# Kernel optimization log

Measured on AMD Instinct MI355X. Metric: run time of the kernel, lower is better.

The kernel has to match this reference:

```python
import jax, jax.numpy as jnp
import numpy as np

KH = KW = 3
PAD = 1
STRIDE = 1
C_IN = 32
C_OUT = 16
H = W = 64
B = 64
H_OUT = (H - KH + 2 * PAD) // STRIDE + 1
W_OUT = (W - KW + 2 * PAD) // STRIDE + 1
S = H_OUT * W_OUT
K = C_IN * KH * KW


def unfold_2d(x):
    # x: [B, C, H, W] -> [B, C*KH*KW, S], torch.nn.functional.unfold ordering
    xp = jnp.pad(x, ((0, 0), (0, 0), (PAD, PAD), (PAD, PAD)))
    patches = []
    for i in range(KH):
        for j in range(KW):
            patches.append(xp[:, :, i:i + H_OUT * STRIDE:STRIDE, j:j + W_OUT * STRIDE:STRIDE])
    u = jnp.stack(patches, axis=2)  # [B, C, KH*KW, H_OUT, W_OUT]
    return u.reshape(x.shape[0], K, S)


def setup_inputs() -> dict:
    key = jax.random.key(0)
    k1, k2, k3 = jax.random.split(key, 3)
    X = jax.random.normal(k1, (B, C_IN, H, W), dtype=jnp.float32)
    # kaiming normal (linear): std = 1/sqrt(fan_in), fan_in = K for each location's GEMM
    weight = jax.random.normal(k2, (S, K, C_OUT), dtype=jnp.float32) / jnp.sqrt(jnp.float32(K))
    # xavier uniform over [H_OUT, W_OUT]
    lim = np.sqrt(6.0 / (H_OUT + W_OUT))
    bias = jax.random.uniform(k3, (H_OUT, W_OUT), dtype=jnp.float32, minval=-lim, maxval=lim)
    return {"X": X, "weight": weight, "bias": bias}


def reference(X, weight, bias):
    ufld = unfold_2d(X)                               # [B, K, S]
    ufld = ufld + bias.reshape(1, 1, -1)              # bias added per-location to patches
    h = jnp.einsum('bks,skc->bcs', ufld, weight)      # per-location unshared GEMM
    return h.reshape(X.shape[0], C_OUT, H_OUT, W_OUT)
```

## Files before the change

### kernel.cpp

```cpp
#include <hip/hip_runtime.h>
#include <stdint.h>
#include <stddef.h>

#define HOUT 64
#define WOUT 64
#define CIN  32
#define COUT 16
#define BATCH 64
#define SLOC 4096
#define KTOT 288
#define HPAD 66

typedef __attribute__((ext_vector_type(8))) short  short8;
typedef __attribute__((ext_vector_type(4))) float  floatx4;

static __device__ __forceinline__ unsigned short f2bf(float f) {
    union { float f; unsigned int u; } v; v.f = f;
    unsigned int u = v.u;
    unsigned int r = (u + 0x7FFFu + ((u >> 16) & 1u)) >> 16;
    return (unsigned short)r;
}

__global__ __launch_bounds__(256) void zero_border_kernel(unsigned short* __restrict__ xt) {
    int bid = blockIdx.x;
    int h1, w1;
    if (bid < 66)       { h1 = 0;  w1 = bid; }
    else if (bid < 132) { h1 = 65; w1 = bid - 66; }
    else { int r = bid - 132; h1 = (r >> 1) + 1; w1 = (r & 1) ? 65 : 0; }
    uint4* dst = (uint4*)(xt + (size_t)(h1 * HPAD + w1) * 2048);
    dst[threadIdx.x] = uint4{0u, 0u, 0u, 0u};
}

__global__ __launch_bounds__(256) void transpose_kernel(const float* __restrict__ X,
                                                        unsigned short* __restrict__ xt) {
    int h = blockIdx.x;
    int b = blockIdx.y;
    int t = threadIdx.x;
    int w  = t >> 2;
    int cg = t & 3;

    const float* xb = X + (((size_t)b * CIN + cg * 8) * HOUT + h) * WOUT + w;
    unsigned short v[8];
#pragma unroll
    for (int j = 0; j < 8; ++j)
        v[j] = f2bf(xb[(size_t)j * HOUT * WOUT]);

    uint4 pack;
    pack.x = (unsigned)v[0] | ((unsigned)v[1] << 16);
    pack.y = (unsigned)v[2] | ((unsigned)v[3] << 16);
    pack.z = (unsigned)v[4] | ((unsigned)v[5] << 16);
    pack.w = (unsigned)v[6] | ((unsigned)v[7] << 16);

    *(uint4*)(xt + (size_t)((h + 1) * HPAD + (w + 1)) * 2048 + b * CIN + cg * 8) = pack;
}

__global__ __launch_bounds__(576) void wprep_kernel(const float* __restrict__ Wg,
                                                    const float* __restrict__ bias,
                                                    uint4* __restrict__ wt,
                                                    float* __restrict__ bsum) {
    __shared__ float red[9][16];
    int s    = blockIdx.x;
    int t    = threadIdx.x >> 6;
    int lane = threadIdx.x & 63;
    int q = lane >> 4, n = lane & 15;

    const float* wb = Wg + (size_t)s * (KTOT * COUT) + (size_t)((8 * q) * 9 + t) * COUT + n;
    float w[8];
#pragma unroll
    for (int j = 0; j < 8; ++j)
        w[j] = wb[(size_t)j * 9 * COUT];

    float csum = 0.f;
    unsigned short h[8];
#pragma unroll
    for (int j = 0; j < 8; ++j) { csum += w[j]; h[j] = f2bf(w[j]); }

    uint4 pack;
    pack.x = (unsigned)h[0] | ((unsigned)h[1] << 16);
    pack.y = (unsigned)h[2] | ((unsigned)h[3] << 16);
    pack.z = (unsigned)h[4] | ((unsigned)h[5] << 16);
    pack.w = (unsigned)h[6] | ((unsigned)h[7] << 16);
    wt[(size_t)(s * 9 + t) * 64 + lane] = pack;

    csum += __shfl_xor(csum, 16, 64);
    csum += __shfl_xor(csum, 32, 64);
    if (lane < 16) red[t][n] = csum;
    __syncthreads();
    if (threadIdx.x < 16) {
        float tot = 0.f;
#pragma unroll
        for (int tt = 0; tt < 9; ++tt) tot += red[tt][threadIdx.x];
        bsum[s * COUT + threadIdx.x] = bias[s] * tot;
    }
}

__global__ __launch_bounds__(256, 4) void varconv_kernel(const unsigned short* __restrict__ xt,
                                                         const uint4* __restrict__ wt,
                                                         const float* __restrict__ bsum,
                                                         float* __restrict__ out) {
    __shared__ float lds[16 * 16 * 16];

    int id = blockIdx.x;
    int lo = id & 7;
    int q4 = (id >> 3) & 3;
    int g  = ((id >> 5) << 3) | lo;
    int s0 = g * 16;
    int y  = s0 >> 6;
    int x0 = s0 & 63;
    int B0 = q4 * 16;

    int lane = threadIdx.x & 63, wv = threadIdx.x >> 6;
    int q = lane >> 4;
    int n = lane & 15;

#pragma unroll
    for (int i = 0; i < 4; ++i) {
        int sl = wv * 4 + i;
        int s  = s0 + sl;
        int x  = x0 + sl;

        const uint4* wf = wt + (size_t)s * 9 * 64 + lane;
        short8 bf[9];
#pragma unroll
        for (int t = 0; t < 9; ++t)
            bf[t] = *(const short8*)(wf + t * 64);

        float badd = bsum[s * COUT + n];

        const unsigned short* ab = xt + (size_t)(B0 + n) * CIN + q * 8;
        short8 af[9];
#pragma unroll
        for (int t = 0; t < 9; ++t) {
            const int cy = t / 3, cx = t % 3;
            af[t] = *(const short8*)(ab + (size_t)((y + cy) * HPAD + (x + cx)) * 2048);
        }

        floatx4 acc = {0.f, 0.f, 0.f, 0.f};
#pragma unroll
        for (int t = 0; t < 9; ++t)
            acc = __builtin_amdgcn_mfma_f32_16x16x32_bf16(af[t], bf[t], acc, 0, 0, 0);

        int slot = q ^ (n & 3);
        floatx4 v = {acc[0] + badd, acc[1] + badd, acc[2] + badd, acc[3] + badd};
        *(floatx4*)&lds[n * 256 + sl * 16 + slot * 4] = v;
    }

    __syncthreads();

    int c   = lane >> 2;
    int slg = lane & 3;
#pragma unroll
    for (int i2 = 0; i2 < 4; ++i2) {
        int ib   = wv * 4 + i2;
        int slot = (ib >> 2) ^ (c & 3);
        float o0[4];
#pragma unroll
        for (int e = 0; e < 4; ++e)
            o0[e] = lds[c * 256 + (slg * 4 + e) * 16 + slot * 4 + (ib & 3)];
        floatx4 o = {o0[0], o0[1], o0[2], o0[3]};
        *(floatx4*)(out + ((size_t)((B0 + ib) * COUT + c)) * SLOC + s0 + slg * 4) = o;
    }
}

extern "C" void kernel_launch(void* const* d_in, const int* in_sizes, int n_in,
                              void* d_out, int out_size, void* d_ws, size_t ws_size,
                              hipStream_t stream) {
    const float* X    = (const float*)d_in[0];
    const float* Wg   = (const float*)d_in[1];
    const float* bias = (const float*)d_in[2];
    float* out = (float*)d_out;

    unsigned short* xt = (unsigned short*)d_ws;
    uint4* wt   = (uint4*)((char*)d_ws + 17842176);
    float* bsum = (float*)((char*)d_ws + 17842176 + 37748736);

    zero_border_kernel<<<260, 256, 0, stream>>>(xt);
    transpose_kernel<<<dim3(64, 64), 256, 0, stream>>>(X, xt);
    wprep_kernel<<<SLOC, 576, 0, stream>>>(Wg, bias, wt, bsum);
    varconv_kernel<<<1024, 256, 0, stream>>>(xt, wt, bsum, out);
}
```

Measured before the change: 165.2 us.

## Fuse border-zero, transpose and weight-prep kernels into one prep kernel; pad LDS rows

Merges the three preprocessing kernels (border zeroing, input transpose to bf16, weight packing with bias sums) into a single 1024-block kernel. Each block now does four transpose units and one wave per weight location, with the bias column sum reduced by wave shuffles instead of an LDS reduction. The goal is to cut launch overhead and the tiny-block inefficiency of the separate kernels. Separately, the output-staging LDS tile gets a padded stride (324/20) to reduce bank conflicts. Each thread now does more serial work, so the prep kernel has fewer waves in flight to hide memory latency.

```diff
diff --git a/kernel.cpp b/kernel.cpp
--- a/kernel.cpp
+++ b/kernel.cpp
@@ -21,76 +21,74 @@
     return (unsigned short)r;
 }
 
-__global__ __launch_bounds__(256) void zero_border_kernel(unsigned short* __restrict__ xt) {
-    int bid = blockIdx.x;
-    int h1, w1;
-    if (bid < 66)       { h1 = 0;  w1 = bid; }
-    else if (bid < 132) { h1 = 65; w1 = bid - 66; }
-    else { int r = bid - 132; h1 = (r >> 1) + 1; w1 = (r & 1) ? 65 : 0; }
-    uint4* dst = (uint4*)(xt + (size_t)(h1 * HPAD + w1) * 2048);
-    dst[threadIdx.x] = uint4{0u, 0u, 0u, 0u};
-}
+__global__ __launch_bounds__(256, 4) void prep_kernel(const float* __restrict__ X,
+                                                      const float* __restrict__ Wg,
+                                                      const float* __restrict__ bias,
+                                                      unsigned short* __restrict__ xt,
+                                                      uint4* __restrict__ wt,
+                                                      float* __restrict__ bsum) {
+    const int id   = blockIdx.x;
+    const int tid  = threadIdx.x;
+    const int lane = tid & 63;
+    const int wv   = tid >> 6;
 
-__global__ __launch_bounds__(256) void transpose_kernel(const float* __restrict__ X,
-                                                        unsigned short* __restrict__ xt) {
-    int h = blockIdx.x;
-    int b = blockIdx.y;
-    int t = threadIdx.x;
-    int w  = t >> 2;
-    int cg = t & 3;
+    if (id < 260) {
+        int h1, w1;
+        if (id < 66)       { h1 = 0;  w1 = id; }
+        else if (id < 132) { h1 = 65; w1 = id - 66; }
+        else { int r = id - 132; h1 = (r >> 1) + 1; w1 = (r & 1) ? 65 : 0; }
+        ((uint4*)(xt + (size_t)(h1 * HPAD + w1) * 2048))[tid] = uint4{0u, 0u, 0u, 0u};
+    }
 
-    const float* xb = X + (((size_t)b * CIN + cg * 8) * HOUT + h) * WOUT + w;
-    unsigned short v[8];
+    {
+        const int w   = tid >> 2;
+        const int cg8 = (tid & 3) * 8;
 #pragma unroll
-    for (int j = 0; j < 8; ++j)
-        v[j] = f2bf(xb[(size_t)j * HOUT * WOUT]);
+        for (int u = 0; u < 4; ++u) {
+            const int unit = id * 4 + u;
+            const int h = unit >> 6, b = unit & 63;
+            const float* xb = X + (((size_t)b * CIN + cg8) * HOUT + h) * WOUT + w;
+            unsigned short v[8];
+#pragma unroll
+            for (int j = 0; j < 8; ++j)
+                v[j] = f2bf(xb[(size_t)j * HOUT * WOUT]);
+            uint4 pack;
+            pack.x = (unsigned)v[0] | ((unsigned)v[1] << 16);
+            pack.y = (unsigned)v[2] | ((unsigned)v[3] << 16);
+            pack.z = (unsigned)v[4] | ((unsigned)v[5] << 16);
+            pack.w = (unsigned)v[6] | ((unsigned)v[7] << 16);
+            *(uint4*)(xt + (size_t)((h + 1) * HPAD + (w + 1)) * 2048 + b * CIN + cg8) = pack;
+        }
+    }
 
-    uint4 pack;
-    pack.x = (unsigned)v[0] | ((unsigned)v[1] << 16);
-    pack.y = (unsigned)v[2] | ((unsigned)v[3] << 16);
-    pack.z = (unsigned)v[4] | ((unsigned)v[5] << 16);
-    pack.w = (unsigned)v[6] | ((unsigned)v[7] << 16);
+    {
+        const int lo = id & 7;
+        const int q4 = (id >> 3) & 3;
+        const int g  = ((id >> 5) << 3) | lo;
+        const int s  = g * 16 + q4 * 4 + wv;
+        const int q = lane >> 4, n = lane & 15;
 
-    *(uint4*)(xt + (size_t)((h + 1) * HPAD + (w + 1)) * 2048 + b * CIN + cg * 8) = pack;
-}
-
-__global__ __launch_bounds__(576) void wprep_kernel(const float* __restrict__ Wg,
-                                                    const float* __restrict__ bias,
-                                                    uint4* __restrict__ wt,
-                                                    float* __restrict__ bsum) {
-    __shared__ float red[9][16];
-    int s    = blockIdx.x;
-    int t    = threadIdx.x >> 6;
-    int lane = threadIdx.x & 63;
-    int q = lane >> 4, n = lane & 15;
-
-    const float* wb = Wg + (size_t)s * (KTOT * COUT) + (size_t)((8 * q) * 9 + t) * COUT + n;
-    float w[8];
+        const float* wb = Wg + (size_t)s * (KTOT * COUT) + (size_t)(8 * q) * 9 * COUT + n;
+        float csum = 0.f;
 #pragma unroll
-    for (int j = 0; j < 8; ++j)
-        w[j] = wb[(size_t)j * 9 * COUT];
-
-    float csum = 0.f;
-    unsigned short h[8];
+        for (int t = 0; t < 9; ++t) {
+            float w[8];
 #pragma unroll
-    for (int j = 0; j < 8; ++j) { csum += w[j]; h[j] = f2bf(w[j]); }
-
-    uint4 pack;
-    pack.x = (unsigned)h[0] | ((unsigned)h[1] << 16);
-    pack.y = (unsigned)h[2] | ((unsigned)h[3] << 16);
-    pack.z = (unsigned)h[4] | ((unsigned)h[5] << 16);
-    pack.w = (unsigned)h[6] | ((unsigned)h[7] << 16);
-    wt[(size_t)(s * 9 + t) * 64 + lane] = pack;
-
-    csum += __shfl_xor(csum, 16, 64);
-    csum += __shfl_xor(csum, 32, 64);
-    if (lane < 16) red[t][n] = csum;
-    __syncthreads();
-    if (threadIdx.x < 16) {
-        float tot = 0.f;
+            for (int j = 0; j < 8; ++j)
+                w[j] = wb[(size_t)t * COUT + (size_t)j * 9 * COUT];
+            unsigned short hh[8];
 #pragma unroll
-        for (int tt = 0; tt < 9; ++tt) tot += red[tt][threadIdx.x];
-        bsum[s * COUT + threadIdx.x] = bias[s] * tot;
+            for (int j = 0; j < 8; ++j) { csum += w[j]; hh[j] = f2bf(w[j]); }
+            uint4 pack;
+            pack.x = (unsigned)hh[0] | ((unsigned)hh[1] << 16);
+            pack.y = (unsigned)hh[2] | ((unsigned)hh[3] << 16);
+            pack.z = (unsigned)hh[4] | ((unsigned)hh[5] << 16);
+            pack.w = (unsigned)hh[6] | ((unsigned)hh[7] << 16);
+            wt[(size_t)(s * 9 + t) * 64 + lane] = pack;
+        }
+        csum += __shfl_xor(csum, 16, 64);
+        csum += __shfl_xor(csum, 32, 64);
+        if (lane < 16) bsum[s * COUT + n] = bias[s] * csum;
     }
 }
 
@@ -98,7 +96,7 @@
                                                          const uint4* __restrict__ wt,
                                                          const float* __restrict__ bsum,
                                                          float* __restrict__ out) {
-    __shared__ float lds[16 * 16 * 16];
+    __shared__ float lds[16 * 324];
 
     int id = blockIdx.x;
     int lo = id & 7;
@@ -142,7 +140,7 @@
 
         int slot = q ^ (n & 3);
         floatx4 v = {acc[0] + badd, acc[1] + badd, acc[2] + badd, acc[3] + badd};
-        *(floatx4*)&lds[n * 256 + sl * 16 + slot * 4] = v;
+        *(floatx4*)&lds[n * 324 + sl * 20 + slot * 4] = v;
     }
 
     __syncthreads();
@@ -156,7 +154,7 @@
         float o0[4];
 #pragma unroll
         for (int e = 0; e < 4; ++e)
-            o0[e] = lds[c * 256 + (slg * 4 + e) * 16 + slot * 4 + (ib & 3)];
+            o0[e] = lds[c * 324 + (slg * 4 + e) * 20 + slot * 4 + (ib & 3)];
         floatx4 o = {o0[0], o0[1], o0[2], o0[3]};
         *(floatx4*)(out + ((size_t)((B0 + ib) * COUT + c)) * SLOC + s0 + slg * 4) = o;
     }
@@ -174,8 +172,6 @@
     uint4* wt   = (uint4*)((char*)d_ws + 17842176);
     float* bsum = (float*)((char*)d_ws + 17842176 + 37748736);
 
-    zero_border_kernel<<<260, 256, 0, stream>>>(xt);
-    transpose_kernel<<<dim3(64, 64), 256, 0, stream>>>(X, xt);
-    wprep_kernel<<<SLOC, 576, 0, stream>>>(Wg, bias, wt, bsum);
+    prep_kernel<<<1024, 256, 0, stream>>>(X, Wg, bias, xt, wt, bsum);
     varconv_kernel<<<1024, 256, 0, stream>>>(xt, wt, bsum, out);
 }
```

New measurement: 166.0 us. No clear change (+0.5%).
